# Performance work log

Measured on AMD Instinct MI355X. Metric: run time of the kernel, lower is better.

The kernel has to match this reference:

```python
import jax, jax.numpy as jnp
import numpy as np


def setup_inputs() -> dict:
    key = jax.random.key(0)
    ks = jax.random.split(key, 6)
    B, T, D, Dg, U = 64, 2048, 256, 256, 256
    return {
        "x": jax.random.normal(ks[0], (B, T, D), dtype=jnp.float32),
        "g": jax.random.normal(ks[1], (B, 1, Dg), dtype=jnp.float32),
        "W": jax.random.normal(ks[2], (D, U), dtype=jnp.float32) * 0.05,
        "Wg": jax.random.normal(ks[3], (Dg, U), dtype=jnp.float32) * 0.05,
        "b": jax.random.normal(ks[4], (U,), dtype=jnp.float32) * 0.05,
        "v": jax.random.normal(ks[5], (U,), dtype=jnp.float32) * 0.05,
    }


def reference(x, g, W, Wg, b, v):
    # x: [B, T, D], g: [B, 1, Dg]
    g2 = g[:, 0, :]                                  # [B, Dg]
    atten_g = (g2 @ Wg)[:, None, :]                  # [B, 1, U]
    # activation is linear (default activation=None in Keras)
    et = jnp.einsum('btd,du->btu', x, W) + atten_g + b   # [B, T, U]
    scores = jnp.einsum('btu,u->bt', et, v)          # [B, T]
    at = jax.nn.softmax(scores, axis=-1)             # softmax over sequence
    return jnp.einsum('bt,btd->bd', at, x)           # weighted sum pooling
```

## Files before the change

kernel.cpp:

```cpp
#include <hip/hip_runtime.h>

#define B 64
#define T 2048
#define D 256
#define U 256
#define NC 32
#define TC (T / NC)

typedef float fx4 __attribute__((ext_vector_type(4)));

#define WS_WV   0
#define WS_L    (WS_WV + 256)
#define WS_O    (WS_L + B * NC)

__global__ __launch_bounds__(256) void k_wv(const float* __restrict__ W,
                                            const float* __restrict__ v,
                                            float* __restrict__ wv) {
    int tid = threadIdx.x;
    int dl  = tid >> 4;
    int sub = tid & 15;
    int d   = (blockIdx.x << 4) + dl;
    const float4* Wr = (const float4*)(W + (long long)d * U);
    const float4* v4 = (const float4*)v;
    float acc = 0.f;
    #pragma unroll
    for (int u = 0; u < 4; ++u) {
        float4 w  = Wr[sub + (u << 4)];
        float4 vv = v4[sub + (u << 4)];
        acc += w.x * vv.x + w.y * vv.y + w.z * vv.z + w.w * vv.w;
    }
    #pragma unroll
    for (int off = 1; off < 16; off <<= 1)
        acc += __shfl_xor(acc, off, 64);
    if (sub == 0) wv[d] = acc;
}

__global__ __launch_bounds__(256) void k_fused(const float* __restrict__ x,
                                               const float* __restrict__ wv,
                                               float* __restrict__ pL,
                                               float* __restrict__ pO) {
    int b = blockIdx.x >> 5;
    int c = blockIdx.x & (NC - 1);
    int l = threadIdx.x & 63;
    int q = threadIdx.x >> 6;

    float4 w4 = ((const float4*)wv)[l];
    const fx4* xb =
        (const fx4*)(x + ((long long)b * T + (long long)c * TC) * D);

    float lsum = 0.f;
    float4 acc = {0.f, 0.f, 0.f, 0.f};

    for (int t = q; t < TC; t += 8) {
        fx4 xa = __builtin_nontemporal_load(&xb[(long long)t * 64 + l]);
        fx4 xc = __builtin_nontemporal_load(&xb[(long long)(t + 4) * 64 + l]);
        float sa = xa.x * w4.x + xa.y * w4.y + xa.z * w4.z + xa.w * w4.w;
        float sc = xc.x * w4.x + xc.y * w4.y + xc.z * w4.z + xc.w * w4.w;
        #pragma unroll
        for (int off = 1; off < 64; off <<= 1) {
            sa += __shfl_xor(sa, off, 64);
            sc += __shfl_xor(sc, off, 64);
        }
        float pa = __expf(sa);
        float pc = __expf(sc);
        lsum += pa + pc;
        acc.x = fmaf(pa, xa.x, fmaf(pc, xc.x, acc.x));
        acc.y = fmaf(pa, xa.y, fmaf(pc, xc.y, acc.y));
        acc.z = fmaf(pa, xa.z, fmaf(pc, xc.z, acc.z));
        acc.w = fmaf(pa, xa.w, fmaf(pc, xc.w, acc.w));
    }

    __shared__ float4 redO[4][64];
    __shared__ float redL[4];
    redO[q][l] = acc;
    if (l == 0) redL[q] = lsum;
    __syncthreads();
    if (q == 0) {
        float4 a0 = redO[0][l], a1 = redO[1][l], a2 = redO[2][l], a3 = redO[3][l];
        float4 r;
        r.x = (a0.x + a1.x) + (a2.x + a3.x);
        r.y = (a0.y + a1.y) + (a2.y + a3.y);
        r.z = (a0.z + a1.z) + (a2.z + a3.z);
        r.w = (a0.w + a1.w) + (a2.w + a3.w);
        ((float4*)(pO + (long long)blockIdx.x * D))[l] = r;
        if (l == 0)
            pL[blockIdx.x] = (redL[0] + redL[1]) + (redL[2] + redL[3]);
    }
}

__global__ __launch_bounds__(256) void k_combine(const float* __restrict__ pL,
                                                 const float* __restrict__ pO,
                                                 float* __restrict__ out) {
    int b = blockIdx.x;
    int d = threadIdx.x;
    float denom = 0.f, acc = 0.f;
    #pragma unroll
    for (int c = 0; c < NC; ++c) {
        denom += pL[b * NC + c];
        acc   += pO[((long long)(b * NC + c)) * D + d];
    }
    out[(long long)b * D + d] = acc / denom;
}

extern "C" void kernel_launch(void* const* d_in, const int* in_sizes, int n_in,
                              void* d_out, int out_size, void* d_ws, size_t ws_size,
                              hipStream_t stream) {
    const float* x = (const float*)d_in[0];
    const float* W = (const float*)d_in[2];
    const float* v = (const float*)d_in[5];
    float* ws = (float*)d_ws;
    float* wv = ws + WS_WV;
    float* pL = ws + WS_L;
    float* pO = ws + WS_O;
    float* out = (float*)d_out;

    k_wv<<<16, 256, 0, stream>>>(W, v, wv);
    k_fused<<<B * NC, 256, 0, stream>>>(x, wv, pL, pO);
    k_combine<<<B, 256, 0, stream>>>(pL, pO, out);
}
```

Measured before the change: 191.3 us.

## Split wavefront into 16-lane groups so each group handles a separate row

```diff
diff --git a/kernel.cpp b/kernel.cpp
--- a/kernel.cpp
+++ b/kernel.cpp
@@ -12,6 +12,10 @@
 #define WS_WV   0
 #define WS_L    (WS_WV + 256)
 #define WS_O    (WS_L + B * NC)
+
+__device__ __forceinline__ float dot4(fx4 a, fx4 b) {
+    return fmaf(a.x, b.x, fmaf(a.y, b.y, fmaf(a.z, b.z, a.w * b.w)));
+}
 
 __global__ __launch_bounds__(256) void k_wv(const float* __restrict__ W,
                                             const float* __restrict__ v,
@@ -43,46 +47,74 @@
     int c = blockIdx.x & (NC - 1);
     int l = threadIdx.x & 63;
     int q = threadIdx.x >> 6;
+    int s16 = l & 15;
+    int g = l >> 4;
 
-    float4 w4 = ((const float4*)wv)[l];
+    const fx4* wv4 = (const fx4*)wv;
+    fx4 w0 = wv4[s16];
+    fx4 w1 = wv4[s16 + 16];
+    fx4 w2 = wv4[s16 + 32];
+    fx4 w3 = wv4[s16 + 48];
+
     const fx4* xb =
         (const fx4*)(x + ((long long)b * T + (long long)c * TC) * D);
+    const fx4* xr = xb + ((long long)(q * 16 + g)) * 64 + s16;
 
     float lsum = 0.f;
-    float4 acc = {0.f, 0.f, 0.f, 0.f};
+    fx4 a0 = {0,0,0,0}, a1 = {0,0,0,0}, a2 = {0,0,0,0}, a3 = {0,0,0,0};
 
-    for (int t = q; t < TC; t += 8) {
-        fx4 xa = __builtin_nontemporal_load(&xb[(long long)t * 64 + l]);
-        fx4 xc = __builtin_nontemporal_load(&xb[(long long)(t + 4) * 64 + l]);
-        float sa = xa.x * w4.x + xa.y * w4.y + xa.z * w4.z + xa.w * w4.w;
-        float sc = xc.x * w4.x + xc.y * w4.y + xc.z * w4.z + xc.w * w4.w;
+    #pragma unroll 2
+    for (int quad = 0; quad < 4; ++quad) {
+        const fx4* p = xr + quad * 4 * 64;
+        fx4 x0 = __builtin_nontemporal_load(p);
+        fx4 x1 = __builtin_nontemporal_load(p + 16);
+        fx4 x2 = __builtin_nontemporal_load(p + 32);
+        fx4 x3 = __builtin_nontemporal_load(p + 48);
+        float s = dot4(x0, w0) + dot4(x1, w1) + dot4(x2, w2) + dot4(x3, w3);
         #pragma unroll
-        for (int off = 1; off < 64; off <<= 1) {
-            sa += __shfl_xor(sa, off, 64);
-            sc += __shfl_xor(sc, off, 64);
-        }
-        float pa = __expf(sa);
-        float pc = __expf(sc);
-        lsum += pa + pc;
-        acc.x = fmaf(pa, xa.x, fmaf(pc, xc.x, acc.x));
-        acc.y = fmaf(pa, xa.y, fmaf(pc, xc.y, acc.y));
-        acc.z = fmaf(pa, xa.z, fmaf(pc, xc.z, acc.z));
-        acc.w = fmaf(pa, xa.w, fmaf(pc, xc.w, acc.w));
+        for (int off = 1; off < 16; off <<= 1)
+            s += __shfl_xor(s, off, 64);
+        float pe = __expf(s);
+        lsum += pe;
+        a0.x = fmaf(pe, x0.x, a0.x); a0.y = fmaf(pe, x0.y, a0.y);
+        a0.z = fmaf(pe, x0.z, a0.z); a0.w = fmaf(pe, x0.w, a0.w);
+        a1.x = fmaf(pe, x1.x, a1.x); a1.y = fmaf(pe, x1.y, a1.y);
+        a1.z = fmaf(pe, x1.z, a1.z); a1.w = fmaf(pe, x1.w, a1.w);
+        a2.x = fmaf(pe, x2.x, a2.x); a2.y = fmaf(pe, x2.y, a2.y);
+        a2.z = fmaf(pe, x2.z, a2.z); a2.w = fmaf(pe, x2.w, a2.w);
+        a3.x = fmaf(pe, x3.x, a3.x); a3.y = fmaf(pe, x3.y, a3.y);
+        a3.z = fmaf(pe, x3.z, a3.z); a3.w = fmaf(pe, x3.w, a3.w);
     }
 
-    __shared__ float4 redO[4][64];
+    #pragma unroll
+    for (int off = 16; off < 64; off <<= 1) {
+        a0.x += __shfl_xor(a0.x, off, 64); a0.y += __shfl_xor(a0.y, off, 64);
+        a0.z += __shfl_xor(a0.z, off, 64); a0.w += __shfl_xor(a0.w, off, 64);
+        a1.x += __shfl_xor(a1.x, off, 64); a1.y += __shfl_xor(a1.y, off, 64);
+        a1.z += __shfl_xor(a1.z, off, 64); a1.w += __shfl_xor(a1.w, off, 64);
+        a2.x += __shfl_xor(a2.x, off, 64); a2.y += __shfl_xor(a2.y, off, 64);
+        a2.z += __shfl_xor(a2.z, off, 64); a2.w += __shfl_xor(a2.w, off, 64);
+        a3.x += __shfl_xor(a3.x, off, 64); a3.y += __shfl_xor(a3.y, off, 64);
+        a3.z += __shfl_xor(a3.z, off, 64); a3.w += __shfl_xor(a3.w, off, 64);
+        lsum += __shfl_xor(lsum, off, 64);
+    }
+
+    __shared__ fx4 redO[4][16][4];
     __shared__ float redL[4];
-    redO[q][l] = acc;
-    if (l == 0) redL[q] = lsum;
+    if (l < 16) {
+        redO[q][s16][0] = a0;
+        redO[q][s16][1] = a1;
+        redO[q][s16][2] = a2;
+        redO[q][s16][3] = a3;
+        if (l == 0) redL[q] = lsum;
+    }
     __syncthreads();
     if (q == 0) {
-        float4 a0 = redO[0][l], a1 = redO[1][l], a2 = redO[2][l], a3 = redO[3][l];
-        float4 r;
-        r.x = (a0.x + a1.x) + (a2.x + a3.x);
-        r.y = (a0.y + a1.y) + (a2.y + a3.y);
-        r.z = (a0.z + a1.z) + (a2.z + a3.z);
-        r.w = (a0.w + a1.w) + (a2.w + a3.w);
-        ((float4*)(pO + (long long)blockIdx.x * D))[l] = r;
+        int k = l >> 4;
+        fx4 r0 = redO[0][s16][k], r1 = redO[1][s16][k];
+        fx4 r2 = redO[2][s16][k], r3 = redO[3][s16][k];
+        fx4 r = (r0 + r1) + (r2 + r3);
+        ((fx4*)(pO + (long long)blockIdx.x * D))[s16 + 16 * k] = r;
         if (l == 0)
             pL[blockIdx.x] = (redL[0] + redL[1]) + (redL[2] + redL[3]);
     }
```

Result: no change. 192.8 us (median of 2 runs) (+0.8%).
